# Performance work log

Measured on AMD Instinct MI355X. Metric: run time of the kernel, lower is better.

## Reference

```python
import jax, jax.numpy as jnp
import numpy as np
from jax import lax

ALIGNED_H = 7
ALIGNED_W = 7
SPATIAL_SCALE = 0.125
B, C, H, W = 4, 512, 96, 96
R = 512
IMG = 768  # image resolution (features are image/8)


def setup_inputs() -> dict:
    key = jax.random.key(0)
    k1, k2, k3, k4, k5, k6 = jax.random.split(key, 6)
    features = jax.random.normal(k1, (B, C, H, W), dtype=jnp.float32)
    # realistic rois: [batch_idx, x1, y1, x2, y2] in image coordinates
    bi = jax.random.randint(k2, (R,), 0, B).astype(jnp.float32)
    cx = jax.random.uniform(k3, (R,), minval=32.0, maxval=float(IMG - 32))
    cy = jax.random.uniform(k4, (R,), minval=32.0, maxval=float(IMG - 32))
    bw = jax.random.uniform(k5, (R,), minval=16.0, maxval=256.0)
    bh = jax.random.uniform(k6, (R,), minval=16.0, maxval=256.0)
    x1 = jnp.clip(cx - bw / 2, 0.0, IMG - 1.0)
    x2 = jnp.clip(cx + bw / 2, 0.0, IMG - 1.0)
    y1 = jnp.clip(cy - bh / 2, 0.0, IMG - 1.0)
    y2 = jnp.clip(cy + bh / 2, 0.0, IMG - 1.0)
    rois = jnp.stack([bi, x1, y1, x2, y2], axis=1)
    return {"features": features, "rois": rois}


def _roi_align_ada(features, rois, ah, aw, scale):
    """RoIAlignAda: per output pixel, average of a 3x3 adaptive-stride grid of
    bilinear samples centered at the bin point (RT-MDNet ROIAlignAdaForward)."""
    b, c, h, w = features.shape
    r = rois.shape[0]
    batch_ind = rois[:, 0].astype(jnp.int32)
    x1 = rois[:, 1] * scale
    y1 = rois[:, 2] * scale
    x2 = rois[:, 3] * scale
    y2 = rois[:, 4] * scale
    roi_w = jnp.maximum(x2 - x1, 0.0)
    roi_h = jnp.maximum(y2 - y1, 0.0)
    bin_h = roi_h / (ah - 1.0)  # [R]
    bin_w = roi_w / (aw - 1.0)
    ph = jnp.arange(ah, dtype=jnp.float32)
    pw = jnp.arange(aw, dtype=jnp.float32)
    hc = y1[:, None] + ph[None, :] * bin_h[:, None]  # [R, AH] bin centers
    wc = x1[:, None] + pw[None, :] * bin_w[:, None]  # [R, AW]
    stride_h = jnp.maximum(1.0, jnp.round(bin_h / 3.0))  # [R]
    stride_w = jnp.maximum(1.0, jnp.round(bin_w / 3.0))

    center_ok = ((hc >= 0) & (hc < h))[:, :, None] & ((wc >= 0) & (wc < w))[:, None, :]  # [R,AH,AW]

    # flatten spatial for gathers: [B*H*W, C]
    f = features.transpose(0, 2, 3, 1).reshape(b * h * w, c)
    base = batch_ind[:, None, None] * (h * w)  # [R,1,1]

    acc = jnp.zeros((r, ah, aw, c), dtype=features.dtype)
    cnt = jnp.zeros((r, ah, aw), dtype=features.dtype)
    for sh in (-1.0, 0.0, 1.0):
        for sw in (-1.0, 0.0, 1.0):
            ch = hc + sh * stride_h[:, None]  # [R,AH]
            cw = wc + sw * stride_w[:, None]  # [R,AW]
            valid = ((ch >= 0) & (ch < h))[:, :, None] & ((cw >= 0) & (cw < w))[:, None, :]
            hs = jnp.clip(jnp.floor(ch), 0.0, h - 2.0)
            ws = jnp.clip(jnp.floor(cw), 0.0, w - 2.0)
            hr = (ch - hs)[:, :, None]  # [R,AH,1]
            wr = (cw - ws)[:, None, :] * jnp.ones((r, ah, aw), features.dtype)[:, :1, :1]  # broadcast helper
            wr = (cw - ws)[:, None, :]  # [R,1,AW]
            hsi = hs.astype(jnp.int32)[:, :, None]  # [R,AH,1]
            wsi = ws.astype(jnp.int32)[:, None, :]  # [R,1,AW]
            ul = base + hsi * w + wsi  # [R,AH,AW]
            v = (f[ul] * ((1.0 - hr) * (1.0 - wr))[..., None]
                 + f[ul + 1] * ((1.0 - hr) * wr)[..., None]
                 + f[ul + w] * (hr * (1.0 - wr))[..., None]
                 + f[ul + w + 1] * (hr * wr)[..., None])  # [R,AH,AW,C]
            acc = acc + jnp.where(valid[..., None], v, 0.0)
            cnt = cnt + valid.astype(features.dtype)

    out = jnp.where(center_ok[..., None], acc / jnp.maximum(cnt, 1.0)[..., None], 0.0)
    return out.transpose(0, 3, 1, 2)  # [R, C, AH, AW]


def reference(features, rois):
    x = _roi_align_ada(features, rois, ALIGNED_H + 4, ALIGNED_W + 4, SPATIAL_SCALE)  # [R,C,11,11]
    # fused 3x3 stride-2 max pool -> [R, C, 5, 5]
    out = lax.reduce_window(x, -jnp.inf, lax.max,
                            window_dimensions=(1, 1, 3, 3),
                            window_strides=(1, 1, 2, 2),
                            padding='VALID')
    return out
```

## Files before the change

### kernel.cpp

```cpp
#include <hip/hip_runtime.h>
#include <stdint.h>

typedef unsigned short u16;
typedef unsigned int   u32;

#define Bn 4
#define Cc 512
#define Hh 96
#define Ww 96
#define HWc (Hh*Ww)
#define AH 11
#define Rr 512
#define CP (Cc/2)

__device__ __forceinline__ u16 f2bf(float f){
  u32 u = __float_as_uint(f);
  u += 0x7fffu + ((u>>16)&1u);
  return (u16)(u>>16);
}
__device__ __forceinline__ u32 pk2(float a, float b){
  return (u32)f2bf(a) | ((u32)f2bf(b)<<16);
}

__global__ __launch_bounds__(256)
void transpose_kernel(const float* __restrict__ in, u32* __restrict__ out){
  __shared__ u32 tile[128*64];
  const int t = threadIdx.x;
  const int hw0 = blockIdx.x*128, c0 = blockIdx.y*128, b = blockIdx.z;
  {
    const int q = t & 31, cp0 = t >> 5;
    const float* ib = in + ((size_t)(b*Cc + c0))*HWc + hw0 + 4*q;
    #pragma unroll
    for (int p=0;p<8;++p){
      const int cp = cp0 + p*8;
      const float* pa = ib + (size_t)(2*cp)*HWc;
      float4 A = *(const float4*)pa;
      float4 B = *(const float4*)(pa + HWc);
      const int cs = cp ^ q;
      tile[(4*q+0)*64 + cs] = pk2(A.x,B.x);
      tile[(4*q+1)*64 + cs] = pk2(A.y,B.y);
      tile[(4*q+2)*64 + cs] = pk2(A.z,B.z);
      tile[(4*q+3)*64 + cs] = pk2(A.w,B.w);
    }
  }
  __syncthreads();
  {
    const int l = t & 63, wv = t >> 6;
    u32* ob = out + ((size_t)b*HWc + hw0)*CP + (c0>>1) + l;
    #pragma unroll
    for (int k=0;k<32;++k){
      const int hw = wv*32 + k;
      ob[(size_t)hw*CP] = tile[hw*64 + (l ^ (hw>>2))];
    }
  }
}

__device__ __forceinline__ float2 bilin(const u32 v[16], const float cw[4], const float rw[4]){
  float ax=0.0f, ay=0.0f;
  #pragma unroll
  for (int i=0;i<4;++i){
    float cx=0.0f, cy=0.0f;
    #pragma unroll
    for (int j=0;j<4;++j){
      u32 d = v[i*4+j];
      cx = fmaf(cw[j], __uint_as_float(d<<16),           cx);
      cy = fmaf(cw[j], __uint_as_float(d & 0xffff0000u), cy);
    }
    ax = fmaf(rw[i], cx, ax);
    ay = fmaf(rw[i], cy, ay);
  }
  return make_float2(ax, ay);
}

__global__ __launch_bounds__(128)
void roi_align_max_nhwc(const u32* __restrict__ feat,
                        const float* __restrict__ rois,
                        float* __restrict__ out)
{
  __shared__ __align__(16) int4   s_ro[AH];
  __shared__ __align__(16) float4 s_rw[AH];
  __shared__ __align__(16) int4   s_co[AH];
  __shared__ __align__(16) float4 s_cw[AH];
  __shared__ int s_b;
  __shared__ __align__(16) float s_out[256*25];

  const int t    = threadIdx.x;
  const int r    = blockIdx.x >> 1;
  const int half = blockIdx.x & 1;

  if (t == 0){
    int b = (int)rois[r*5+0];
    s_b = min(max(b, 0), Bn-1);
  }

  if (t < AH || (t >= 64 && t < 64+AH)){
    const bool isrow = (t < AH);
    const int  p = isrow ? t : t-64;
    const float* rp = rois + r*5;
    const float c1 = rp[isrow?2:1], c2 = rp[isrow?4:3];
    float lo  = __fmul_rn(c1, 0.125f);
    float hi  = __fmul_rn(c2, 0.125f);
    float ext = fmaxf(__fsub_rn(hi,lo), 0.0f);
    float bin = __fdiv_rn(ext, 10.0f);
    float ctr = __fadd_rn(lo, __fmul_rn((float)p, bin));
    float strd = fmaxf(1.0f, rintf(__fdiv_rn(bin, 3.0f)));
    bool ok = (ctr >= 0.0f) && (ctr < 96.0f);
    int rws[6]; float wts[6]; int nv=0;
    #pragma unroll
    for (int s=0;s<3;++s){
      float cc = __fadd_rn(ctr, __fmul_rn((float)(s-1), strd));
      bool vv = (cc >= 0.0f) && (cc < 96.0f);
      float fl = fminf(fmaxf(floorf(cc),0.0f),94.0f);
      float fr = __fsub_rn(cc, fl);
      int ri = (int)fl;
      rws[2*s]=ri; rws[2*s+1]=ri+1;
      wts[2*s]  = vv ? __fsub_rn(1.0f,fr) : 0.0f;
      wts[2*s+1]= vv ? fr : 0.0f;
      nv += vv?1:0;
    }
    float sc = ok ? (1.0f/(float)nv) : 0.0f;
    int cr[4]={0,0,0,0}; float cwv[4]={0.0f,0.0f,0.0f,0.0f}; int n=0;
    for (int k=0;k<6;++k){
      float wk=wts[k]; if (wk==0.0f) continue;
      int rr=rws[k]; bool fnd=false;
      for (int j=0;j<n;++j) if (cr[j]==rr){ cwv[j]+=wk; fnd=true; break; }
      if (!fnd && n<4){ cr[n]=rr; cwv[n]=wk; ++n; }
    }
    const int mul = isrow ? (Ww*CP*4) : (CP*4);
    if (isrow){
      s_ro[p] = make_int4(cr[0]*mul, cr[1]*mul, cr[2]*mul, cr[3]*mul);
      s_rw[p] = make_float4(cwv[0]*sc, cwv[1]*sc, cwv[2]*sc, cwv[3]*sc);
    } else {
      s_co[p] = make_int4(cr[0]*mul, cr[1]*mul, cr[2]*mul, cr[3]*mul);
      s_cw[p] = make_float4(cwv[0]*sc, cwv[1]*sc, cwv[2]*sc, cwv[3]*sc);
    }
  }
  __syncthreads();

  const char* fb = (const char*)(feat + (size_t)s_b*((size_t)HWc*CP));
  const int tb4 = (half*128 + t)*4;

  int   vo[AH][4]; float cwr[AH][4];
  #pragma unroll
  for (int pw=0; pw<AH; ++pw){
    int4 c4 = s_co[pw]; float4 w4 = s_cw[pw];
    vo[pw][0]=tb4+c4.x; vo[pw][1]=tb4+c4.y; vo[pw][2]=tb4+c4.z; vo[pw][3]=tb4+c4.w;
    cwr[pw][0]=w4.x; cwr[pw][1]=w4.y; cwr[pw][2]=w4.z; cwr[pw][3]=w4.w;
  }

  float2 awin[5];
  #pragma unroll 1
  for (int ph=0; ph<AH; ++ph){
    int4   r4 = s_ro[ph];
    float4 w4 = s_rw[ph];
    const char* r0 = fb + __builtin_amdgcn_readfirstlane(r4.x);
    const char* r1 = fb + __builtin_amdgcn_readfirstlane(r4.y);
    const char* r2 = fb + __builtin_amdgcn_readfirstlane(r4.z);
    const char* r3 = fb + __builtin_amdgcn_readfirstlane(r4.w);
    const float rw_[4] = {w4.x, w4.y, w4.z, w4.w};
    float2 binr[AH];
    u32 va[16], vb[16], vc[16];

#define LDV(dst, PW) do{                              \
    dst[ 0] = *(const u32*)(r0 + vo[PW][0]);          \
    dst[ 1] = *(const u32*)(r0 + vo[PW][1]);          \
    dst[ 2] = *(const u32*)(r0 + vo[PW][2]);          \
    dst[ 3] = *(const u32*)(r0 + vo[PW][3]);          \
    dst[ 4] = *(const u32*)(r1 + vo[PW][0]);          \
    dst[ 5] = *(const u32*)(r1 + vo[PW][1]);          \
    dst[ 6] = *(const u32*)(r1 + vo[PW][2]);          \
    dst[ 7] = *(const u32*)(r1 + vo[PW][3]);          \
    dst[ 8] = *(const u32*)(r2 + vo[PW][0]);          \
    dst[ 9] = *(const u32*)(r2 + vo[PW][1]);          \
    dst[10] = *(const u32*)(r2 + vo[PW][2]);          \
    dst[11] = *(const u32*)(r2 + vo[PW][3]);          \
    dst[12] = *(const u32*)(r3 + vo[PW][0]);          \
    dst[13] = *(const u32*)(r3 + vo[PW][1]);          \
    dst[14] = *(const u32*)(r3 + vo[PW][2]);          \
    dst[15] = *(const u32*)(r3 + vo[PW][3]);          \
  }while(0)
#define CMP(src, PW) binr[PW] = bilin(src, cwr[PW], rw_)

    LDV(va, 0); LDV(vb, 1); LDV(vc, 2);
    CMP(va, 0); LDV(va, 3);
    CMP(vb, 1); LDV(vb, 4);
    CMP(vc, 2); LDV(vc, 5);
    CMP(va, 3); LDV(va, 6);
    CMP(vb, 4); LDV(vb, 7);
    CMP(vc, 5); LDV(vc, 8);
    CMP(va, 6); LDV(va, 9);
    CMP(vb, 7); LDV(vb, 10);
    CMP(vc, 8);
    CMP(va, 9);
    CMP(vb, 10);
#undef LDV
#undef CMP

    float2 rm[5];
    #pragma unroll
    for (int ox=0; ox<5; ++ox){
      rm[ox].x = fmaxf(fmaxf(binr[2*ox].x, binr[2*ox+1].x), binr[2*ox+2].x);
      rm[ox].y = fmaxf(fmaxf(binr[2*ox].y, binr[2*ox+1].y), binr[2*ox+2].y);
    }
    if (ph == 0){
      #pragma unroll
      for (int ox=0; ox<5; ++ox) awin[ox] = rm[ox];
    } else if (ph & 1){
      #pragma unroll
      for (int ox=0; ox<5; ++ox){
        awin[ox].x = fmaxf(awin[ox].x, rm[ox].x);
        awin[ox].y = fmaxf(awin[ox].y, rm[ox].y);
      }
    } else {
      const int oy = (ph-2) >> 1;
      #pragma unroll
      for (int ox=0; ox<5; ++ox){
        s_out[(2*t  )*25 + oy*5 + ox] = fmaxf(awin[ox].x, rm[ox].x);
        s_out[(2*t+1)*25 + oy*5 + ox] = fmaxf(awin[ox].y, rm[ox].y);
        awin[ox] = rm[ox];
      }
    }
  }
  __syncthreads();

  float4* dst = (float4*)(out + (size_t)r*(Cc*25) + half*(256*25));
  const float4* src = (const float4*)s_out;
  for (int k=t; k<(256*25)/4; k+=128) dst[k]=src[k];
}

__global__ __launch_bounds__(512, 1)
void roi_align_max_nchw(const float* __restrict__ feat,
                        const float* __restrict__ rois,
                        float* __restrict__ out)
{
  __shared__ int   s_roff[AH][6];
  __shared__ float s_rw  [AH][6];
  __shared__ int   s_coff[AH][6];
  __shared__ float s_cw  [AH][6];
  __shared__ int   s_b;
  __shared__ __align__(16) float s_out[Cc*25];

  const int t = threadIdx.x;
  const int r = blockIdx.x;

  if (t < AH*6){
    ((float*)s_rw)[t] = 0.0f;  ((int*)s_roff)[t] = 0;
    ((float*)s_cw)[t] = 0.0f;  ((int*)s_coff)[t] = 0;
  }
  if (t == 0){
    int b = (int)rois[r*5+0];
    s_b = min(max(b, 0), Bn-1);
  }
  __syncthreads();

  if (t < AH || (t >= 64 && t < 64+AH)){
    const bool isrow = (t < AH);
    const int  p = isrow ? t : t-64;
    const float* rp = rois + r*5;
    const float c1 = rp[isrow?2:1], c2 = rp[isrow?4:3];
    float lo  = __fmul_rn(c1, 0.125f);
    float hi  = __fmul_rn(c2, 0.125f);
    float ext = fmaxf(__fsub_rn(hi,lo), 0.0f);
    float bin = __fdiv_rn(ext, 10.0f);
    float ctr = __fadd_rn(lo, __fmul_rn((float)p, bin));
    float strd = fmaxf(1.0f, rintf(__fdiv_rn(bin, 3.0f)));
    bool ok = (ctr >= 0.0f) && (ctr < 96.0f);
    int rws[6]; float wts[6]; int nv=0;
    #pragma unroll
    for (int s=0;s<3;++s){
      float cc = __fadd_rn(ctr, __fmul_rn((float)(s-1), strd));
      bool vv = (cc >= 0.0f) && (cc < 96.0f);
      float fl = fminf(fmaxf(floorf(cc),0.0f),94.0f);
      float fr = __fsub_rn(cc, fl);
      int ri = (int)fl;
      rws[2*s]=ri; rws[2*s+1]=ri+1;
      wts[2*s]  = vv ? __fsub_rn(1.0f,fr) : 0.0f;
      wts[2*s+1]= vv ? fr : 0.0f;
      nv += vv?1:0;
    }
    float sc = ok ? (1.0f/(float)nv) : 0.0f;
    int cr[6]; float cw[6]; int n=0;
    for (int k=0;k<6;++k){
      float wk=wts[k]; if (wk==0.0f) continue;
      if (n>0 && cr[n-1]==rws[k]) cw[n-1]+=wk;
      else { cr[n]=rws[k]; cw[n]=wk; ++n; }
    }
    const int mul = isrow ? Ww : 1;
    for (int k=0;k<n;++k){
      int off = cr[k]*mul;
      float wv = cw[k]*sc;
      if (isrow){ s_roff[p][k]=off; s_rw[p][k]=wv; }
      else      { s_coff[p][k]=off; s_cw[p][k]=wv; }
    }
  }
  __syncthreads();

  const float* f0 = feat + ((size_t)s_b*Cc + t)*HWc;
  float awin[5];
  for (int ph=0; ph<AH; ++ph){
    float binrow[AH];
    #pragma unroll
    for (int pw=0; pw<AH; ++pw){
      float acc = 0.0f;
      #pragma unroll
      for (int ai=0; ai<6; ++ai){
        float ra = s_rw[ph][ai];
        if (ra == 0.0f) continue;
        int ro = s_roff[ph][ai];
        #pragma unroll
        for (int bi=0; bi<6; ++bi){
          float cb = s_cw[pw][bi];
          if (cb == 0.0f) continue;
          acc = fmaf(ra*cb, f0[ro + s_coff[pw][bi]], acc);
        }
      }
      binrow[pw] = acc;
    }
    float rm[5];
    #pragma unroll
    for (int ox=0; ox<5; ++ox)
      rm[ox] = fmaxf(fmaxf(binrow[2*ox], binrow[2*ox+1]), binrow[2*ox+2]);
    if (ph == 0){
      #pragma unroll
      for (int ox=0; ox<5; ++ox) awin[ox] = rm[ox];
    } else if (ph & 1){
      #pragma unroll
      for (int ox=0; ox<5; ++ox) awin[ox] = fmaxf(awin[ox], rm[ox]);
    } else {
      int oy = (ph-2) >> 1;
      #pragma unroll
      for (int ox=0; ox<5; ++ox){
        s_out[t*25 + oy*5 + ox] = fmaxf(awin[ox], rm[ox]);
        awin[ox] = rm[ox];
      }
    }
  }
  __syncthreads();

  float4* dst = (float4*)(out + (size_t)r*(Cc*25));
  const float4* src = (const float4*)s_out;
  for (int k=t; k<(Cc*25)/4; k+=512) dst[k]=src[k];
}

extern "C" void kernel_launch(void* const* d_in, const int* in_sizes, int n_in,
                              void* d_out, int out_size, void* d_ws, size_t ws_size,
                              hipStream_t stream)
{
  (void)in_sizes; (void)n_in; (void)out_size;
  const float* feat = (const float*)d_in[0];
  const float* rois = (const float*)d_in[1];
  float* out = (float*)d_out;
  const size_t need = (size_t)Bn*HWc*Cc*sizeof(u16);
  if (ws_size >= need){
    u32* ws = (u32*)d_ws;
    dim3 g(HWc/128, Cc/128, Bn);
    transpose_kernel<<<g, 256, 0, stream>>>(feat, ws);
    roi_align_max_nhwc<<<Rr*2, 128, 0, stream>>>(ws, rois, out);
  } else {
    roi_align_max_nchw<<<Rr, 512, 0, stream>>>(feat, rois, out);
  }
}
```

Baseline: 167.9 us.

## Sort ROIs by batch index and interleave blocks across batches for cache locality

Adds a small counting-sort kernel that groups ROI indices by batch image, then remaps block IDs so concurrently running blocks spread across the four batch images and ROIs of the same image are scheduled near each other. The aim is better L2/MALL reuse of the transposed bf16 feature map when many ROIs of one image read overlapping regions. It costs an extra tiny kernel launch and some index arithmetic per block, and it only takes effect if the workspace has 4 KB of room beyond the transposed features.

```diff
diff --git a/kernel.cpp b/kernel.cpp
--- a/kernel.cpp
+++ b/kernel.cpp
@@ -55,6 +55,25 @@
   }
 }
 
+__global__ __launch_bounds__(512)
+void roi_sort(const float* __restrict__ rois, int* __restrict__ idx){
+  __shared__ int cnt[4], off[4], cur[4];
+  const int t = threadIdx.x;
+  int b = min(max((int)rois[t*5], 0), Bn-1);
+  if (t < 4){ cnt[t] = 0; }
+  __syncthreads();
+  atomicAdd(&cnt[b], 1);
+  __syncthreads();
+  if (t == 0){
+    int o = 0;
+    for (int i=0;i<4;++i){ off[i]=o; cur[i]=o; o+=cnt[i]; }
+  }
+  __syncthreads();
+  int pos = atomicAdd(&cur[b], 1);
+  idx[8+pos] = t;
+  if (t < 4){ idx[t] = cnt[t]; idx[4+t] = off[t]; }
+}
+
 __device__ __forceinline__ float2 bilin(const u32 v[16], const float cw[4], const float rw[4]){
   float ax=0.0f, ay=0.0f;
   #pragma unroll
@@ -75,7 +94,8 @@
 __global__ __launch_bounds__(128)
 void roi_align_max_nhwc(const u32* __restrict__ feat,
                         const float* __restrict__ rois,
-                        float* __restrict__ out)
+                        float* __restrict__ out,
+                        const int* __restrict__ idx)
 {
   __shared__ __align__(16) int4   s_ro[AH];
   __shared__ __align__(16) float4 s_rw[AH];
@@ -84,9 +104,32 @@
   __shared__ int s_b;
   __shared__ __align__(16) float s_out[256*25];
 
-  const int t    = threadIdx.x;
-  const int r    = blockIdx.x >> 1;
-  const int half = blockIdx.x & 1;
+  const int t   = threadIdx.x;
+  const int bid = blockIdx.x;
+
+  int r, half;
+  if (idx){
+    const int k = bid & 7;
+    const int j = bid >> 3;
+    const int b = k >> 1;
+    half = k & 1;
+    const int cntb = idx[b];
+    if (j < cntb && j < 128){
+      r = idx[8 + idx[4+b] + j];
+    } else {
+      int dr = 0;
+      for (int b2=0; b2<b; ++b2) dr += max(0, 128 - idx[b2]);
+      dr += j - min(cntb, 128);
+      int acc = 0; r = 0;
+      for (int b2=0; b2<4; ++b2){
+        int ex = max(0, idx[b2] - 128);
+        if (dr < acc + ex){ r = idx[8 + idx[4+b2] + 128 + (dr - acc)]; break; }
+        acc += ex;
+      }
+    }
+  } else {
+    r = bid >> 1; half = bid & 1;
+  }
 
   if (t == 0){
     int b = (int)rois[r*5+0];
@@ -353,9 +396,14 @@
   const size_t need = (size_t)Bn*HWc*Cc*sizeof(u16);
   if (ws_size >= need){
     u32* ws = (u32*)d_ws;
+    int* idx = nullptr;
+    if (ws_size >= need + 4096){
+      idx = (int*)((char*)d_ws + need);
+      roi_sort<<<1, 512, 0, stream>>>(rois, idx);
+    }
     dim3 g(HWc/128, Cc/128, Bn);
     transpose_kernel<<<g, 256, 0, stream>>>(feat, ws);
-    roi_align_max_nhwc<<<Rr*2, 128, 0, stream>>>(ws, rois, out);
+    roi_align_max_nhwc<<<Rr*2, 128, 0, stream>>>(ws, rois, out, idx);
   } else {
     roi_align_max_nchw<<<Rr, 512, 0, stream>>>(feat, rois, out);
   }
```

Result: faster. 164.0 us (-2.3%).
